# Kernel optimization log

Hardware: AMD Instinct MI355X
Metric: run time of the kernel (lower is better)

The kernel has to match this reference:

```python
import jax, jax.numpy as jnp
import numpy as np

BS, S, D, H, HS, HSEL, L = 32, 512, 512, 8, 2, 4, 6
DK = D // H  # 64
HD = H - HS  # dynamic heads


def setup_inputs() -> dict:
    key = jax.random.key(0)
    ks = jax.random.split(key, 10)
    w = lambda k, shape: jax.random.normal(k, shape, dtype=jnp.float32) * 0.02
    return {
        'q_embed_data': jax.random.normal(ks[0], (BS, S, D), jnp.float32),
        'qa_embed_data': jax.random.normal(ks[1], (BS, S, D), jnp.float32),
        # stacked per-layer params (torch Linear convention: W[out,in], y = x@W.T+b)
        'Wq': w(ks[2], (L, D, D)), 'bq': jnp.zeros((L, D), jnp.float32),
        'Wv': w(ks[3], (L, D, D)), 'bv': jnp.zeros((L, D), jnp.float32),
        'Wg': w(ks[4], (L, HD, D)),                      # routing gate, no bias
        'Wo': w(ks[5], (L, D, D)), 'bo': jnp.zeros((L, D), jnp.float32),
        'ln1_g': jnp.ones((L, D), jnp.float32), 'ln1_b': jnp.zeros((L, D), jnp.float32),
        'W1': w(ks[6], (L, D, D)), 'b1': jnp.zeros((L, D), jnp.float32),
        'W2': w(ks[7], (L, D, D)), 'b2': jnp.zeros((L, D), jnp.float32),
        'ln2_g': jnp.ones((L, D), jnp.float32), 'ln2_b': jnp.zeros((L, D), jnp.float32),
    }


def _layer_norm(x, g, b):
    m = x.mean(-1, keepdims=True)
    v = ((x - m) ** 2).mean(-1, keepdims=True)
    return (x - m) * jax.lax.rsqrt(v + 1e-5) * g + b


def _moh_attention(xq, xv, Wq, bq, Wv, bv, Wg, Wo, bo, strict):
    bs, s, d = xq.shape
    q = xq @ Wq.T + bq            # kq_same=True: k = q projection
    v = xv @ Wv.T + bv
    qh = q.reshape(bs, s, H, DK).transpose(0, 2, 1, 3)   # [b,h,s,dk]
    vh = v.reshape(bs, s, H, DK).transpose(0, 2, 1, 3)
    scores = jnp.einsum('bhqd,bhkd->bhqk', qh, qh) / jnp.sqrt(jnp.float32(DK))
    # mask==1 -> causal incl. diag; mask==0 -> strictly causal
    allow = jnp.tril(jnp.ones((s, s), bool), k=-1 if strict else 0)
    scores = jnp.where(allow, scores, jnp.float32(-1e9))
    # pad-zero shift: first query row replaced by zeros -> uniform attention
    scores = scores.at[:, :, 0, :].set(0.0)
    # per-token top-k head routing over dynamic heads
    gates = jax.nn.softmax(q.reshape(bs * s, D) @ Wg.T, axis=-1)  # [bs*s, HD]
    _, idx = jax.lax.top_k(gates, HSEL)
    dmask = jnp.zeros_like(gates).at[jnp.arange(bs * s)[:, None], idx].set(1.0)
    dyn = (gates * dmask).reshape(bs, s, HD)
    routing = jnp.concatenate([jnp.ones((bs, s, HS), gates.dtype), dyn], -1).mean(1)  # [b,H]
    attn = jax.nn.softmax(scores, axis=-1)
    ctx = jnp.einsum('bhqk,bhkd->bhqd', attn, vh) * routing[:, :, None, None]
    out = ctx.transpose(0, 2, 1, 3).reshape(bs, s, D) @ Wo.T + bo
    f = dmask.sum(0)
    P = gates.mean(0)
    balance = jnp.sum((f / (f.sum() + 1e-5)) * (P / (P.sum() + 1e-5)))
    return out, balance


def reference(q_embed_data, qa_embed_data, Wq, bq, Wv, bv, Wg, Wo, bo,
              ln1_g, ln1_b, W1, b1, W2, b2, ln2_g, ln2_b):
    def layer(i, xq, xv, strict):
        a, bl = _moh_attention(xq, xv, Wq[i], bq[i], Wv[i], bv[i], Wg[i], Wo[i], bo[i], strict)
        x = _layer_norm(xq + a, ln1_g[i], ln1_b[i])
        ffn = jax.nn.relu(x @ W1[i].T + b1[i]) @ W2[i].T + b2[i]
        return _layer_norm(x + ffn, ln2_g[i], ln2_b[i]), bl

    y = qa_embed_data
    x = q_embed_data
    # blocks_1: self-attention on y, mask=1
    y, _ = layer(0, y, y, False)
    y, _ = layer(1, y, y, False)
    # blocks_2: alternate mask=1 self-attn / mask=0 cross-attn (values=y)
    x, _ = layer(2, x, x, False)
    x, bl = layer(3, x, y, True)
    x, _ = layer(4, x, x, False)
    x, bl = layer(5, x, y, True)
    return (x, bl)
```

## Files before the change

kernel.cpp:

```cpp
#include <hip/hip_runtime.h>
#include <cstdint>

#define BSZ 32
#define SEQ 512
#define DM  512
#define NH  8
#define DK  64
#define HS_ 2
#define HD_ 6
#define NL  6
#define MROWS (BSZ*SEQ)
#define QVLD 1024
#define SCL 0.18033688011112043f

typedef unsigned short bf16_t;
typedef __attribute__((ext_vector_type(4))) float f32x4;
typedef __attribute__((ext_vector_type(8))) short bf16x8;
typedef __attribute__((ext_vector_type(8))) unsigned short u16x8;

#define DEV static __device__ __forceinline__

DEV float bf2f(bf16_t b) {
  unsigned int u = ((unsigned int)b) << 16;
  float f; __builtin_memcpy(&f, &u, 4); return f;
}
DEV bf16_t f2b(float f) {
  unsigned int u; __builtin_memcpy(&u, &f, 4);
  unsigned int r = (u + 0x7fffu + ((u >> 16) & 1u)) >> 16;
  return (bf16_t)r;
}
DEV void unp2(unsigned int w, float& a, float& b) {
  unsigned int ua = w << 16, ub = w & 0xffff0000u;
  __builtin_memcpy(&a, &ua, 4); __builtin_memcpy(&b, &ub, 4);
}
DEV unsigned cvtpk(float lo, float hi) {
  unsigned r;
  asm("v_cvt_pk_bf16_f32 %0, %1, %2" : "=v"(r) : "v"(lo), "v"(hi));
  return r;
}

DEV void gload_lds16(const bf16_t* g, bf16_t* l) {
  __builtin_amdgcn_global_load_lds(
      (const __attribute__((address_space(1))) void*)g,
      (__attribute__((address_space(3))) void*)l, 16, 0, 0);
}

DEV bf16x8 scale_q(bf16x8 v) {
  u16x8 u;
  __builtin_memcpy(&u, &v, 16);
  unsigned w[4];
#pragma unroll
  for (int e = 0; e < 4; ++e)
    w[e] = cvtpk(bf2f(u[2 * e]) * SCL, bf2f(u[2 * e + 1]) * SCL);
  bf16x8 r;
  __builtin_memcpy(&r, w, 16);
  return r;
}

__global__ __launch_bounds__(256) void f2b2_kernel(
    const float* __restrict__ s0, const float* __restrict__ s1,
    bf16_t* __restrict__ d0, bf16_t* __restrict__ d1) {
  const float* s = blockIdx.y ? s1 : s0;
  bf16_t* d = blockIdx.y ? d1 : d0;
  const int i = blockIdx.x * 256 + threadIdx.x;
  float4 v = reinterpret_cast<const float4*>(s)[i];
  ushort4 o;
  o.x = f2b(v.x); o.y = f2b(v.y); o.z = f2b(v.z); o.w = f2b(v.w);
  reinterpret_cast<ushort4*>(d)[i] = o;
}

__global__ __launch_bounds__(256) void f2bw_kernel(
    const float* __restrict__ s0, const float* __restrict__ s1,
    const float* __restrict__ s2, const float* __restrict__ s3,
    const float* __restrict__ s4, bf16_t* __restrict__ dst) {
  const float* srcs[5] = {s0, s1, s2, s3, s4};
  const float* s = srcs[blockIdx.y];
  bf16_t* d = dst + (size_t)blockIdx.y * ((size_t)NL * DM * DM);
  const int i = blockIdx.x * 256 + threadIdx.x;
  float4 v = reinterpret_cast<const float4*>(s)[i];
  ushort4 o;
  o.x = f2b(v.x); o.y = f2b(v.y); o.z = f2b(v.z); o.w = f2b(v.w);
  reinterpret_cast<ushort4*>(d)[i] = o;
}

__global__ __launch_bounds__(256) void gemm_qv(
    const bf16_t* __restrict__ A0, const bf16_t* __restrict__ A1,
    const bf16_t* __restrict__ W0, const bf16_t* __restrict__ W1,
    const float* __restrict__ b0, const float* __restrict__ b1,
    bf16_t* __restrict__ Yb) {
  const int K = 512;
  const int lin = blockIdx.y * 8 + blockIdx.x;
  const int swz = (lin & 7) * 128 + (lin >> 3);
  const int bn = swz & 7, bm = swz >> 3;
  const int tid = threadIdx.x, wid = tid >> 6, lane = tid & 63;
  const int wr = wid >> 1, wc = wid & 1;
  __shared__ __align__(16) bf16_t As[128 * 64];
  __shared__ __align__(16) bf16_t Bs[128 * 64];

  const bool hi = bn >= 4;
  const bf16_t* Asel = hi ? A1 : A0;
  const bf16_t* Wsel = hi ? (W1 - (size_t)512 * K) : W0;
  const float* bsel = hi ? (b1 - 512) : b0;

  f32x4 acc[4][4];
#pragma unroll
  for (int m = 0; m < 4; ++m)
#pragma unroll
    for (int n = 0; n < 4; ++n) acc[m][n] = f32x4{0.f, 0.f, 0.f, 0.f};

  const int lrow = lane & 15, lko = (lane >> 4) * 8;
  const int sr = wid * 8 + (lane >> 3), scol = (lane & 7) * 8;
  const size_t arow0 = (size_t)bm * 128, brow0 = (size_t)bn * 128;

  for (int k0 = 0; k0 < K; k0 += 64) {
#pragma unroll
    for (int i = 0; i < 4; ++i) {
      gload_lds16(Asel + (arow0 + i * 32 + sr) * K + k0 + scol, &As[(i * 4 + wid) * 512]);
      gload_lds16(Wsel + (brow0 + i * 32 + sr) * K + k0 + scol, &Bs[(i * 4 + wid) * 512]);
    }
    __syncthreads();
    bf16x8 af[4][2], bw[4][2];
#pragma unroll
    for (int m = 0; m < 4; ++m)
#pragma unroll
      for (int ks = 0; ks < 2; ++ks)
        af[m][ks] = *reinterpret_cast<const bf16x8*>(
            &As[(wr * 64 + m * 16 + lrow) * 64 + ks * 32 + lko]);
#pragma unroll
    for (int n = 0; n < 4; ++n)
#pragma unroll
      for (int ks = 0; ks < 2; ++ks)
        bw[n][ks] = *reinterpret_cast<const bf16x8*>(
            &Bs[(wc * 64 + n * 16 + lrow) * 64 + ks * 32 + lko]);
    __builtin_amdgcn_s_setprio(1);
#pragma unroll
    for (int ks = 0; ks < 2; ++ks)
#pragma unroll
      for (int m = 0; m < 4; ++m)
#pragma unroll
        for (int n = 0; n < 4; ++n)
          acc[m][n] = __builtin_amdgcn_mfma_f32_16x16x32_bf16(af[m][ks], bw[n][ks], acc[m][n], 0, 0, 0);
    __builtin_amdgcn_s_setprio(0);
    __syncthreads();
  }

  const int r0 = bm * 128 + wr * 64 + (lane >> 4) * 4;
  const int c0 = bn * 128 + wc * 64 + lrow;
#pragma unroll
  for (int n = 0; n < 4; ++n) {
    const int col = c0 + n * 16;
    const float bc = bsel[col];
#pragma unroll
    for (int m = 0; m < 4; ++m)
#pragma unroll
      for (int j = 0; j < 4; ++j)
        Yb[(size_t)(r0 + m * 16 + j) * QVLD + col] = f2b(acc[m][n][j] + bc);
  }
}

template <bool RELU>
__global__ __launch_bounds__(256) void gemm_n512(
    const bf16_t* __restrict__ A, const bf16_t* __restrict__ W,
    const float* __restrict__ bias, bf16_t* __restrict__ Yb) {
  const int K = 512;
  const int lin = blockIdx.y * 4 + blockIdx.x;
  const int swz = (lin & 7) * 128 + (lin >> 3);
  const int bn = swz & 3, bm = swz >> 2;
  const int tid = threadIdx.x, wid = tid >> 6, lane = tid & 63;
  const int wr = wid >> 1, wc = wid & 1;
  __shared__ __align__(16) bf16_t As[64 * 64];
  __shared__ __align__(16) bf16_t Bs[128 * 64];

  f32x4 acc[2][4];
#pragma unroll
  for (int m = 0; m < 2; ++m)
#pragma unroll
    for (int n = 0; n < 4; ++n) acc[m][n] = f32x4{0.f, 0.f, 0.f, 0.f};

  const int lrow = lane & 15, lko = (lane >> 4) * 8;
  const int sr = wid * 8 + (lane >> 3), scol = (lane & 7) * 8;
  const size_t arow0 = (size_t)bm * 64, brow0 = (size_t)bn * 128;

  for (int k0 = 0; k0 < K; k0 += 64) {
#pragma unroll
    for (int i = 0; i < 2; ++i)
      gload_lds16(A + (arow0 + i * 32 + sr) * K + k0 + scol, &As[(i * 4 + wid) * 512]);
#pragma unroll
    for (int i = 0; i < 4; ++i)
      gload_lds16(W + (brow0 + i * 32 + sr) * K + k0 + scol, &Bs[(i * 4 + wid) * 512]);
    __syncthreads();
    bf16x8 af[2][2], bw[4][2];
#pragma unroll
    for (int m = 0; m < 2; ++m)
#pragma unroll
      for (int ks = 0; ks < 2; ++ks)
        af[m][ks] = *reinterpret_cast<const bf16x8*>(
            &As[(wr * 32 + m * 16 + lrow) * 64 + ks * 32 + lko]);
#pragma unroll
    for (int n = 0; n < 4; ++n)
#pragma unroll
      for (int ks = 0; ks < 2; ++ks)
        bw[n][ks] = *reinterpret_cast<const bf16x8*>(
            &Bs[(wc * 64 + n * 16 + lrow) * 64 + ks * 32 + lko]);
    __builtin_amdgcn_s_setprio(1);
#pragma unroll
    for (int ks = 0; ks < 2; ++ks)
#pragma unroll
      for (int m = 0; m < 2; ++m)
#pragma unroll
        for (int n = 0; n < 4; ++n)
          acc[m][n] = __builtin_amdgcn_mfma_f32_16x16x32_bf16(af[m][ks], bw[n][ks], acc[m][n], 0, 0, 0);
    __builtin_amdgcn_s_setprio(0);
    __syncthreads();
  }

  const int r0 = bm * 64 + wr * 32 + (lane >> 4) * 4;
  const int c0 = bn * 128 + wc * 64 + lrow;
#pragma unroll
  for (int n = 0; n < 4; ++n) {
    const int col = c0 + n * 16;
    const float bc = bias[col];
#pragma unroll
    for (int m = 0; m < 2; ++m)
#pragma unroll
      for (int j = 0; j < 4; ++j) {
        float v = acc[m][n][j] + bc;
        if (RELU) v = fmaxf(v, 0.f);
        Yb[(size_t)(r0 + m * 16 + j) * DM + col] = f2b(v);
      }
  }
}

__global__ __launch_bounds__(256) void gates_kernel(
    const bf16_t* __restrict__ qv, const float* __restrict__ Wg,
    float* __restrict__ rdyn, float* __restrict__ fP) {
  __shared__ float wg_s[HD_ * DM];
  __shared__ float blk[4][18];
  const int tid = threadIdx.x, wid = tid >> 6, lane = tid & 63;
  for (int i = tid; i < HD_ * DM / 4; i += 256)
    reinterpret_cast<float4*>(wg_s)[i] = reinterpret_cast<const float4*>(Wg)[i];
  __syncthreads();
  const int bb = blockIdx.x >> 3;
  const int t0 = (blockIdx.x & 7) * 64 + wid * 16;
  float fs[6] = {0, 0, 0, 0, 0, 0}, ps[6] = {0, 0, 0, 0, 0, 0}, rs[6] = {0, 0, 0, 0, 0, 0};
  for (int it = 0; it < 16; ++it) {
    const int tok = bb * SEQ + t0 + it;
    uint4 u = reinterpret_cast<const uint4*>(qv + (size_t)tok * QVLD)[lane];
    float x[8];
    unp2(u.x, x[0], x[1]); unp2(u.y, x[2], x[3]);
    unp2(u.z, x[4], x[5]); unp2(u.w, x[6], x[7]);
    float g[6];
#pragma unroll
    for (int j = 0; j < 6; ++j) {
      float p = 0.f;
#pragma unroll
      for (int e = 0; e < 8; ++e) p = fmaf(x[e], wg_s[j * DM + lane * 8 + e], p);
#pragma unroll
      for (int off = 32; off; off >>= 1) p += __shfl_xor(p, off);
      g[j] = p;
    }
    float mx = g[0];
#pragma unroll
    for (int j = 1; j < 6; ++j) mx = fmaxf(mx, g[j]);
    float se = 0.f;
#pragma unroll
    for (int j = 0; j < 6; ++j) { g[j] = __expf(g[j] - mx); se += g[j]; }
    float inv = 1.f / se;
#pragma unroll
    for (int j = 0; j < 6; ++j) g[j] *= inv;
    int d1 = 0;
#pragma unroll
    for (int j = 1; j < 6; ++j)
      if (g[j] < g[d1] || (g[j] == g[d1] && j > d1)) d1 = j;
    int d2 = (d1 == 0) ? 1 : 0;
#pragma unroll
    for (int j = 0; j < 6; ++j) {
      if (j == d1) continue;
      if (g[j] < g[d2] || (g[j] == g[d2] && j > d2)) d2 = j;
    }
#pragma unroll
    for (int j = 0; j < 6; ++j) {
      const bool drop = (j == d1) || (j == d2);
      fs[j] += drop ? 0.f : 1.f;
      ps[j] += g[j];
      rs[j] += drop ? 0.f : g[j];
    }
  }
  if (lane == 0) {
#pragma unroll
    for (int j = 0; j < 6; ++j) {
      blk[wid][j] = fs[j]; blk[wid][6 + j] = ps[j]; blk[wid][12 + j] = rs[j];
    }
  }
  __syncthreads();
  if (tid < 18) {
    float s = blk[0][tid] + blk[1][tid] + blk[2][tid] + blk[3][tid];
    if (tid < 12) atomicAdd(&fP[tid], s);
    else atomicAdd(&rdyn[bb * 6 + (tid - 12)], s * (1.f / 512.f));
  }
}

__global__ __launch_bounds__(256, 2) void fattn_kernel(
    const bf16_t* __restrict__ qv, const float* __restrict__ rdyn,
    bf16_t* __restrict__ ctx, int strict) {
  const int lin = (blockIdx.z * 8 + blockIdx.y) * 2 + blockIdx.x;
  const int swz = (lin & 7) * 64 + (lin >> 3);
  const int bx = swz & 1, h = (swz >> 1) & 7, b = swz >> 4;
  const int tid = threadIdx.x, wid = tid >> 6, lane = tid & 63;
  const int c0 = lane & 15, grp = lane >> 4;
  const int l3 = lane >> 3, c3 = lane & 7;
  const int kidx = lane & 31, dhalf = lane >> 5;

  __shared__ __align__(16) bf16_t Ks[64 * 64];
  __shared__ __align__(16) bf16_t Vt[64 * 72];
  __shared__ __align__(16) bf16_t Ps[4][32 * 64];
  __shared__ float csum[64];

  const bf16_t* qp = qv;
  const bf16_t* vp = qv + 512;
  const float factor = (h < HS_) ? 1.f : rdyn[b * 6 + (h - HS_)];

  const int qtA = bx, qtB = 3 - bx;
  const int qbaseA = qtA * 128 + wid * 32;
  const int qbaseB = qtB * 128 + wid * 32;

  bf16x8 qfA[2][2], qfB[2][2];
#pragma unroll
  for (int nt = 0; nt < 2; ++nt)
#pragma unroll
    for (int ks = 0; ks < 2; ++ks) {
      qfA[nt][ks] = scale_q(*reinterpret_cast<const bf16x8*>(
          qp + ((size_t)(b * SEQ + qbaseA + nt * 16 + c0)) * QVLD + h * DK + ks * 32 + grp * 8));
      qfB[nt][ks] = scale_q(*reinterpret_cast<const bf16x8*>(
          qp + ((size_t)(b * SEQ + qbaseB + nt * 16 + c0)) * QVLD + h * DK + ks * 32 + grp * 8));
    }

  f32x4 accA[2][4], accB[2][4];
#pragma unroll
  for (int m = 0; m < 2; ++m)
#pragma unroll
    for (int d = 0; d < 4; ++d) {
      accA[m][d] = f32x4{0.f, 0.f, 0.f, 0.f};
      accB[m][d] = f32x4{0.f, 0.f, 0.f, 0.f};
    }
  float mA[2] = {-3e38f, -3e38f}, lA[2] = {0.f, 0.f};
  float mB[2] = {-3e38f, -3e38f}, lB[2] = {0.f, 0.f};
  float cs[8] = {0, 0, 0, 0, 0, 0, 0, 0};

  const int lastA = (qbaseA + 31 - strict) >> 6;
  const int lastB = (qbaseB + 31 - strict) >> 6;
  const int ktmax = 2 * qtB + 1;

  auto do_tile = [&](bf16x8 (&qf)[2][2], f32x4 (&acc)[2][4], float (&mreg)[2],
                     float (&lreg)[2], int qbase, bool masked, int kt) {
    const char* KsB = (const char*)Ks;
    bf16x8 kf[4][2];
#pragma unroll
    for (int mt = 0; mt < 4; ++mt)
#pragma unroll
      for (int ks = 0; ks < 2; ++ks)
        kf[mt][ks] = *reinterpret_cast<const bf16x8*>(
            KsB + (mt * 16 + c0) * 128 + 16 * ((4 * ks + grp) ^ (c0 & 7)));
    f32x4 s[4][2];
#pragma unroll
    for (int mt = 0; mt < 4; ++mt)
#pragma unroll
      for (int nt = 0; nt < 2; ++nt) s[mt][nt] = f32x4{0.f, 0.f, 0.f, 0.f};
    __builtin_amdgcn_s_setprio(1);
#pragma unroll
    for (int mt = 0; mt < 4; ++mt)
#pragma unroll
      for (int nt = 0; nt < 2; ++nt)
#pragma unroll
        for (int ks = 0; ks < 2; ++ks)
          s[mt][nt] = __builtin_amdgcn_mfma_f32_16x16x32_bf16(
              kf[mt][ks], qf[nt][ks], s[mt][nt], 0, 0, 0);
    __builtin_amdgcn_s_setprio(0);

    if (masked) {
#pragma unroll
      for (int nt = 0; nt < 2; ++nt) {
        const int q = qbase + nt * 16 + c0;
#pragma unroll
        for (int mt = 0; mt < 4; ++mt)
#pragma unroll
          for (int j = 0; j < 4; ++j) {
            int k = kt * 64 + mt * 16 + grp * 4 + j;
            if (k + strict > q) s[mt][nt][j] = -1e30f;
          }
      }
    }
    float mx[2];
#pragma unroll
    for (int nt = 0; nt < 2; ++nt) {
      float a = fmaxf(s[0][nt][0], s[0][nt][1]);
      a = fmaxf(fmaxf(a, s[0][nt][2]), s[0][nt][3]);
      float bm_ = fmaxf(s[1][nt][0], s[1][nt][1]);
      bm_ = fmaxf(fmaxf(bm_, s[1][nt][2]), s[1][nt][3]);
      float c = fmaxf(s[2][nt][0], s[2][nt][1]);
      c = fmaxf(fmaxf(c, s[2][nt][2]), s[2][nt][3]);
      float d = fmaxf(s[3][nt][0], s[3][nt][1]);
      d = fmaxf(fmaxf(d, s[3][nt][2]), s[3][nt][3]);
      float m_ = fmaxf(fmaxf(a, bm_), fmaxf(c, d));
      m_ = fmaxf(m_, __shfl_xor(m_, 16));
      m_ = fmaxf(m_, __shfl_xor(m_, 32));
      mx[nt] = m_;
    }
    const bool defer = __all((mx[0] - mreg[0] <= 8.f) && (mx[1] - mreg[1] <= 8.f));
    float sc[2];
#pragma unroll
    for (int nt = 0; nt < 2; ++nt) {
      const float mnew = defer ? mreg[nt] : fmaxf(mreg[nt], mx[nt]);
      float ts = 0.f;
#pragma unroll
      for (int mt = 0; mt < 4; ++mt)
#pragma unroll
        for (int j = 0; j < 4; ++j) {
          float pp = exp2f(s[mt][nt][j] - mnew);
          s[mt][nt][j] = pp; ts += pp;
        }
      ts += __shfl_xor(ts, 16);
      ts += __shfl_xor(ts, 32);
      if (defer) {
        lreg[nt] += ts;
      } else {
        sc[nt] = exp2f(mreg[nt] - mnew);
        lreg[nt] = lreg[nt] * sc[nt] + ts;
        mreg[nt] = mnew;
      }
    }
    char* PsB = (char*)(&Ps[wid][0]);
#pragma unroll
    for (int nt = 0; nt < 2; ++nt)
#pragma unroll
      for (int mt = 0; mt < 4; ++mt) {
        uint2 w;
        w.x = cvtpk(s[mt][nt][0], s[mt][nt][1]);
        w.y = cvtpk(s[mt][nt][2], s[mt][nt][3]);
        int row = nt * 16 + c0;
        int off = (row * 128 + mt * 32 + grp * 8) ^ ((c0 & 7) << 4);
        *reinterpret_cast<uint2*>(PsB + off) = w;
      }
    if (!defer) {
#pragma unroll
      for (int mtq = 0; mtq < 2; ++mtq) {
        f32x4 sv;
#pragma unroll
        for (int j = 0; j < 4; ++j) sv[j] = __shfl(sc[mtq], grp * 4 + j);
#pragma unroll
        for (int dt = 0; dt < 4; ++dt) acc[mtq][dt] *= sv;
      }
    }
    bf16x8 pf[2][2], vf2[4][2];
#pragma unroll
    for (int mtq = 0; mtq < 2; ++mtq)
#pragma unroll
      for (int ks = 0; ks < 2; ++ks)
        pf[mtq][ks] = *reinterpret_cast<const bf16x8*>(
            PsB + (mtq * 16 + c0) * 128 + 16 * ((4 * ks + grp) ^ (c0 & 7)));
#pragma unroll
    for (int dt = 0; dt < 4; ++dt)
#pragma unroll
      for (int ks = 0; ks < 2; ++ks)
        vf2[dt][ks] = *reinterpret_cast<const bf16x8*>(
            (const char*)Vt + (dt * 16 + c0) * 144 + ks * 64 + grp * 16);
    __builtin_amdgcn_s_setprio(1);
#pragma unroll
    for (int mtq = 0; mtq < 2; ++mtq)
#pragma unroll
      for (int dt = 0; dt < 4; ++dt)
#pragma unroll
        for (int ks = 0; ks < 2; ++ks)
          acc[mtq][dt] = __builtin_amdgcn_mfma_f32_16x16x32_bf16(
              pf[mtq][ks], vf2[dt][ks], acc[mtq][dt], 0, 0, 0);
    __builtin_amdgcn_s_setprio(0);
  };

  for (int kt = 0; kt <= ktmax; ++kt) {
#pragma unroll
    for (int i = 0; i < 2; ++i) {
      int row = i * 32 + wid * 8 + l3;
      int blk = c3 ^ l3;
      gload_lds16(qp + ((size_t)(b * SEQ + kt * 64 + row)) * QVLD + h * DK + blk * 8,
                  Ks + (i * 32 + wid * 8) * 64);
    }
#pragma unroll
    for (int j = 0; j < 2; ++j) {
      const int d0 = (wid * 2 + j) * 8 + dhalf * 4;
      const bf16_t* src = vp + ((size_t)(b * SEQ + kt * 64 + 2 * kidx)) * QVLD + h * DK + d0;
      ushort4 lo = *reinterpret_cast<const ushort4*>(src);
      ushort4 hv = *reinterpret_cast<const ushort4*>(src + QVLD);
      *reinterpret_cast<unsigned*>(&Vt[(d0 + 0) * 72 + 2 * kidx]) = (unsigned)lo.x | ((unsigned)hv.x << 16);
      *reinterpret_cast<unsigned*>(&Vt[(d0 + 1) * 72 + 2 * kidx]) = (unsigned)lo.y | ((unsigned)hv.y << 16);
      *reinterpret_cast<unsigned*>(&Vt[(d0 + 2) * 72 + 2 * kidx]) = (unsigned)lo.z | ((unsigned)hv.z << 16);
      *reinterpret_cast<unsigned*>(&Vt[(d0 + 3) * 72 + 2 * kidx]) = (unsigned)lo.w | ((unsigned)hv.w << 16);
      if (bx == 0) {
        cs[j * 4 + 0] += bf2f(lo.x) + bf2f(hv.x);
        cs[j * 4 + 1] += bf2f(lo.y) + bf2f(hv.y);
        cs[j * 4 + 2] += bf2f(lo.z) + bf2f(hv.z);
        cs[j * 4 + 3] += bf2f(lo.w) + bf2f(hv.w);
      }
    }
    __syncthreads();
    if (kt <= lastB) do_tile(qfB, accB, mB, lB, qbaseB, kt == lastB, kt);
    if (kt <= lastA) do_tile(qfA, accA, mA, lA, qbaseA, kt == lastA, kt);
    __syncthreads();
  }

  if (bx == 0) {
#pragma unroll
    for (int e = 0; e < 8; ++e)
#pragma unroll
      for (int off = 1; off <= 16; off <<= 1) cs[e] += __shfl_xor(cs[e], off);
    if ((lane & 31) == 0) {
#pragma unroll
      for (int e = 0; e < 8; ++e)
        csum[(wid * 2 + (e >> 2)) * 8 + dhalf * 4 + (e & 3)] = cs[e];
    }
  }
  __syncthreads();
  if (bx == 0 && tid < 64)
    ctx[((size_t)(b * SEQ)) * DM + h * DK + tid] = f2b(csum[tid] * (1.f / 512.f) * factor);

#pragma unroll
  for (int e = 0; e < 2; ++e) {
    const int qbase = e ? qbaseB : qbaseA;
    f32x4 (&acc)[2][4] = e ? accB : accA;
    float (&lreg)[2] = e ? lB : lA;
#pragma unroll
    for (int mtq = 0; mtq < 2; ++mtq) {
      const float inv = factor / lreg[mtq];
      f32x4 iv;
#pragma unroll
      for (int j = 0; j < 4; ++j) iv[j] = __shfl(inv, grp * 4 + j);
#pragma unroll
      for (int j = 0; j < 4; ++j) {
        const int q = qbase + mtq * 16 + grp * 4 + j;
        if (q == 0) continue;
#pragma unroll
        for (int dt = 0; dt < 4; ++dt)
          ctx[((size_t)(b * SEQ + q)) * DM + h * DK + dt * 16 + c0] =
              f2b(acc[mtq][dt][j] * iv[j]);
      }
    }
  }
}

template <int OUT>
__global__ __launch_bounds__(256) void add_ln_kernel(
    const bf16_t* __restrict__ X, const bf16_t* __restrict__ A2,
    const float* __restrict__ gam, const float* __restrict__ bet,
    bf16_t* __restrict__ outb, float* __restrict__ outf) {
  const int wid = threadIdx.x >> 6, lane = threadIdx.x & 63;
  const size_t row = (size_t)blockIdx.x * 4 + wid;
  const size_t base = row * DM + lane * 8;
  uint4 xu = *reinterpret_cast<const uint4*>(X + base);
  uint4 au = *reinterpret_cast<const uint4*>(A2 + base);
  float z[8];
  {
    float p0, p1, q0, q1;
    unp2(xu.x, p0, p1); unp2(au.x, q0, q1); z[0] = p0 + q0; z[1] = p1 + q1;
    unp2(xu.y, p0, p1); unp2(au.y, q0, q1); z[2] = p0 + q0; z[3] = p1 + q1;
    unp2(xu.z, p0, p1); unp2(au.z, q0, q1); z[4] = p0 + q0; z[5] = p1 + q1;
    unp2(xu.w, p0, p1); unp2(au.w, q0, q1); z[6] = p0 + q0; z[7] = p1 + q1;
  }
  float s = 0.f;
#pragma unroll
  for (int e = 0; e < 8; ++e) s += z[e];
#pragma unroll
  for (int off = 32; off; off >>= 1) s += __shfl_xor(s, off);
  const float mean = s * (1.f / 512.f);
  float ss = 0.f;
#pragma unroll
  for (int e = 0; e < 8; ++e) { float d = z[e] - mean; ss += d * d; }
#pragma unroll
  for (int off = 32; off; off >>= 1) ss += __shfl_xor(ss, off);
  const float inv = rsqrtf(ss * (1.f / 512.f) + 1e-5f);
  float4 g0 = *reinterpret_cast<const float4*>(gam + lane * 8);
  float4 g1 = *reinterpret_cast<const float4*>(gam + lane * 8 + 4);
  float4 b0 = *reinterpret_cast<const float4*>(bet + lane * 8);
  float4 b1 = *reinterpret_cast<const float4*>(bet + lane * 8 + 4);
  float o[8];
  o[0] = (z[0] - mean) * inv * g0.x + b0.x;
  o[1] = (z[1] - mean) * inv * g0.y + b0.y;
  o[2] = (z[2] - mean) * inv * g0.z + b0.z;
  o[3] = (z[3] - mean) * inv * g0.w + b0.w;
  o[4] = (z[4] - mean) * inv * g1.x + b1.x;
  o[5] = (z[5] - mean) * inv * g1.y + b1.y;
  o[6] = (z[6] - mean) * inv * g1.z + b1.z;
  o[7] = (z[7] - mean) * inv * g1.w + b1.w;
  if (OUT == 0) {
    uint4 w;
    w.x = (unsigned)f2b(o[0]) | ((unsigned)f2b(o[1]) << 16);
    w.y = (unsigned)f2b(o[2]) | ((unsigned)f2b(o[3]) << 16);
    w.z = (unsigned)f2b(o[4]) | ((unsigned)f2b(o[5]) << 16);
    w.w = (unsigned)f2b(o[6]) | ((unsigned)f2b(o[7]) << 16);
    *reinterpret_cast<uint4*>(outb + base) = w;
  } else {
    float4 f0, f1;
    f0.x = o[0]; f0.y = o[1]; f0.z = o[2]; f0.w = o[3];
    f1.x = o[4]; f1.y = o[5]; f1.z = o[6]; f1.w = o[7];
    *reinterpret_cast<float4*>(outf + base) = f0;
    *reinterpret_cast<float4*>(outf + base + 4) = f1;
  }
}

__global__ void balance_kernel(const float* __restrict__ fP, float* __restrict__ out) {
  if (threadIdx.x == 0 && blockIdx.x == 0) {
    float fs = 0.f, pssum = 0.f, P[6];
    for (int j = 0; j < 6; ++j) {
      fs += fP[j];
      P[j] = fP[6 + j] * (1.f / (float)MROWS);
      pssum += P[j];
    }
    float bal = 0.f;
    for (int j = 0; j < 6; ++j)
      bal += (fP[j] / (fs + 1e-5f)) * (P[j] / (pssum + 1e-5f));
    out[0] = bal;
  }
}

extern "C" void kernel_launch(void* const* d_in, const int* in_sizes, int n_in,
                              void* d_out, int out_size, void* d_ws, size_t ws_size,
                              hipStream_t stream) {
  (void)in_sizes; (void)n_in; (void)out_size; (void)ws_size;
  const float* q_embed  = (const float*)d_in[0];
  const float* qa_embed = (const float*)d_in[1];
  const float* Wq  = (const float*)d_in[2];
  const float* bq  = (const float*)d_in[3];
  const float* Wv  = (const float*)d_in[4];
  const float* bv  = (const float*)d_in[5];
  const float* Wg  = (const float*)d_in[6];
  const float* Wo  = (const float*)d_in[7];
  const float* bo  = (const float*)d_in[8];
  const float* ln1g = (const float*)d_in[9];
  const float* ln1b = (const float*)d_in[10];
  const float* W1  = (const float*)d_in[11];
  const float* b1  = (const float*)d_in[12];
  const float* W2  = (const float*)d_in[13];
  const float* b2  = (const float*)d_in[14];
  const float* ln2g = (const float*)d_in[15];
  const float* ln2b = (const float*)d_in[16];

  char* p = (char*)d_ws;
  auto alloc = [&](size_t bytes) -> char* {
    char* r = p; p += (bytes + 255) & ~(size_t)255; return r;
  };
  const size_t WDE = (size_t)NL * DM * DM;
  const size_t AE  = (size_t)MROWS * DM;
  bf16_t* wall_b = (bf16_t*)alloc(5 * WDE * 2);
  bf16_t* wq_b = wall_b;
  bf16_t* wv_b = wall_b + WDE;
  bf16_t* wo_b = wall_b + 2 * WDE;
  bf16_t* w1_b = wall_b + 3 * WDE;
  bf16_t* w2_b = wall_b + 4 * WDE;
  bf16_t* y_b   = (bf16_t*)alloc(AE * 2);
  bf16_t* x_b   = (bf16_t*)alloc(AE * 2);
  bf16_t* qv_b  = (bf16_t*)alloc((size_t)MROWS * QVLD * 2);
  bf16_t* ctx_b = (bf16_t*)alloc(AE * 2);
  bf16_t* x1_b  = (bf16_t*)alloc(AE * 2);
  bf16_t* tmp_b = (bf16_t*)alloc(AE * 2);
  bf16_t* ffn1_b = (bf16_t*)alloc(AE * 2);
  float* stats = (float*)alloc(NL * (12 + BSZ * 6) * 4);
  float* fPbase = stats;
  float* rdynbase = stats + NL * 12;

  hipMemsetAsync(stats, 0, NL * (12 + BSZ * 6) * 4, stream);

  f2bw_kernel<<<dim3((unsigned)(WDE / 4 / 256), 5), 256, 0, stream>>>(
      Wq, Wv, Wo, W1, W2, wall_b);
  f2b2_kernel<<<dim3((unsigned)(AE / 4 / 256), 2), 256, 0, stream>>>(
      qa_embed, q_embed, y_b, x_b);

  const size_t DD = (size_t)DM * DM;
  dim3 gqv(8, 128), gn5(4, 256);
  float* outx = (float*)d_out;

  auto layer = [&](int i, bf16_t* resb, const bf16_t* xvb, int strict, bool last) {
    float* fP = fPbase + i * 12;
    float* rdyn = rdynbase + i * (BSZ * 6);
    gemm_qv<<<gqv, 256, 0, stream>>>(
        resb, xvb, wq_b + i * DD, wv_b + i * DD, bq + i * DM, bv + i * DM, qv_b);
    gates_kernel<<<MROWS / 64, 256, 0, stream>>>(qv_b, Wg + (size_t)i * HD_ * DM, rdyn, fP);
    fattn_kernel<<<dim3(2, NH, BSZ), 256, 0, stream>>>(qv_b, rdyn, ctx_b, strict);
    gemm_n512<false><<<gn5, 256, 0, stream>>>(ctx_b, wo_b + i * DD, bo + i * DM, tmp_b);
    add_ln_kernel<0><<<MROWS / 4, 256, 0, stream>>>(
        resb, tmp_b, ln1g + i * DM, ln1b + i * DM, x1_b, nullptr);
    gemm_n512<true><<<gn5, 256, 0, stream>>>(x1_b, w1_b + i * DD, b1 + i * DM, ffn1_b);
    gemm_n512<false><<<gn5, 256, 0, stream>>>(ffn1_b, w2_b + i * DD, b2 + i * DM, tmp_b);
    if (last)
      add_ln_kernel<1><<<MROWS / 4, 256, 0, stream>>>(
          x1_b, tmp_b, ln2g + i * DM, ln2b + i * DM, nullptr, outx);
    else
      add_ln_kernel<0><<<MROWS / 4, 256, 0, stream>>>(
          x1_b, tmp_b, ln2g + i * DM, ln2b + i * DM, resb, nullptr);
  };

  layer(0, y_b, y_b, 0, false);
  layer(1, y_b, y_b, 0, false);
  layer(2, x_b, x_b, 0, false);
  layer(3, x_b, y_b, 1, false);
  layer(4, x_b, x_b, 0, false);
  layer(5, x_b, y_b, 1, true);
  balance_kernel<<<1, 64, 0, stream>>>(fPbase + 5 * 12, outx + (size_t)MROWS * DM);
}
```

Baseline: 1.013 ms.

## Split attention into one block per query tile and halve gates block work

The attention kernel used to pair query tiles (t and 3-t) in one block to balance causal work across 512 blocks. It now launches 1024 blocks, one per query tile, each loading K/V only up to its own causal extent. The column-sum for the zero row moves to the qt==3 block. The gates kernel also uses twice as many blocks with half the tokens each. This adds parallelism and shrinks the per-block register footprint, at the cost of load imbalance across blocks and redundant K/V loads between tiles of the same head.

```diff
diff --git a/kernel.cpp b/kernel.cpp
--- a/kernel.cpp
+++ b/kernel.cpp
@@ -240,10 +240,10 @@
   for (int i = tid; i < HD_ * DM / 4; i += 256)
     reinterpret_cast<float4*>(wg_s)[i] = reinterpret_cast<const float4*>(Wg)[i];
   __syncthreads();
-  const int bb = blockIdx.x >> 3;
-  const int t0 = (blockIdx.x & 7) * 64 + wid * 16;
+  const int bb = blockIdx.x >> 4;
+  const int t0 = (blockIdx.x & 15) * 32 + wid * 8;
   float fs[6] = {0, 0, 0, 0, 0, 0}, ps[6] = {0, 0, 0, 0, 0, 0}, rs[6] = {0, 0, 0, 0, 0, 0};
-  for (int it = 0; it < 16; ++it) {
+  for (int it = 0; it < 8; ++it) {
     const int tok = bb * SEQ + t0 + it;
     uint4 u = reinterpret_cast<const uint4*>(qv + (size_t)tok * QVLD)[lane];
     float x[8];
@@ -303,9 +303,8 @@
 __global__ __launch_bounds__(256, 2) void fattn_kernel(
     const bf16_t* __restrict__ qv, const float* __restrict__ rdyn,
     bf16_t* __restrict__ ctx, int strict) {
-  const int lin = (blockIdx.z * 8 + blockIdx.y) * 2 + blockIdx.x;
-  const int swz = (lin & 7) * 64 + (lin >> 3);
-  const int bx = swz & 1, h = (swz >> 1) & 7, b = swz >> 4;
+  const int bh = blockIdx.x, qt = blockIdx.y;
+  const int b = bh >> 3, h = bh & 7;
   const int tid = threadIdx.x, wid = tid >> 6, lane = tid & 63;
   const int c0 = lane & 15, grp = lane >> 4;
   const int l3 = lane >> 3, c3 = lane & 7;
@@ -320,161 +319,27 @@
   const bf16_t* vp = qv + 512;
   const float factor = (h < HS_) ? 1.f : rdyn[b * 6 + (h - HS_)];
 
-  const int qtA = bx, qtB = 3 - bx;
-  const int qbaseA = qtA * 128 + wid * 32;
-  const int qbaseB = qtB * 128 + wid * 32;
-
-  bf16x8 qfA[2][2], qfB[2][2];
+  const int qbase = qt * 128 + wid * 32;
+
+  bf16x8 qf[2][2];
 #pragma unroll
   for (int nt = 0; nt < 2; ++nt)
 #pragma unroll
-    for (int ks = 0; ks < 2; ++ks) {
-      qfA[nt][ks] = scale_q(*reinterpret_cast<const bf16x8*>(
-          qp + ((size_t)(b * SEQ + qbaseA + nt * 16 + c0)) * QVLD + h * DK + ks * 32 + grp * 8));
-      qfB[nt][ks] = scale_q(*reinterpret_cast<const bf16x8*>(
-          qp + ((size_t)(b * SEQ + qbaseB + nt * 16 + c0)) * QVLD + h * DK + ks * 32 + grp * 8));
-    }
-
-  f32x4 accA[2][4], accB[2][4];
+    for (int ks = 0; ks < 2; ++ks)
+      qf[nt][ks] = scale_q(*reinterpret_cast<const bf16x8*>(
+          qp + ((size_t)(b * SEQ + qbase + nt * 16 + c0)) * QVLD + h * DK + ks * 32 + grp * 8));
+
+  f32x4 acc[2][4];
 #pragma unroll
   for (int m = 0; m < 2; ++m)
 #pragma unroll
-    for (int d = 0; d < 4; ++d) {
-      accA[m][d] = f32x4{0.f, 0.f, 0.f, 0.f};
-      accB[m][d] = f32x4{0.f, 0.f, 0.f, 0.f};
-    }
-  float mA[2] = {-3e38f, -3e38f}, lA[2] = {0.f, 0.f};
-  float mB[2] = {-3e38f, -3e38f}, lB[2] = {0.f, 0.f};
+    for (int d = 0; d < 4; ++d) acc[m][d] = f32x4{0.f, 0.f, 0.f, 0.f};
+  float mreg[2] = {-3e38f, -3e38f};
+  float lreg[2] = {0.f, 0.f};
   float cs[8] = {0, 0, 0, 0, 0, 0, 0, 0};
 
-  const int lastA = (qbaseA + 31 - strict) >> 6;
-  const int lastB = (qbaseB + 31 - strict) >> 6;
-  const int ktmax = 2 * qtB + 1;
-
-  auto do_tile = [&](bf16x8 (&qf)[2][2], f32x4 (&acc)[2][4], float (&mreg)[2],
-                     float (&lreg)[2], int qbase, bool masked, int kt) {
-    const char* KsB = (const char*)Ks;
-    bf16x8 kf[4][2];
-#pragma unroll
-    for (int mt = 0; mt < 4; ++mt)
-#pragma unroll
-      for (int ks = 0; ks < 2; ++ks)
-        kf[mt][ks] = *reinterpret_cast<const bf16x8*>(
-            KsB + (mt * 16 + c0) * 128 + 16 * ((4 * ks + grp) ^ (c0 & 7)));
-    f32x4 s[4][2];
-#pragma unroll
-    for (int mt = 0; mt < 4; ++mt)
-#pragma unroll
-      for (int nt = 0; nt < 2; ++nt) s[mt][nt] = f32x4{0.f, 0.f, 0.f, 0.f};
-    __builtin_amdgcn_s_setprio(1);
-#pragma unroll
-    for (int mt = 0; mt < 4; ++mt)
-#pragma unroll
-      for (int nt = 0; nt < 2; ++nt)
-#pragma unroll
-        for (int ks = 0; ks < 2; ++ks)
-          s[mt][nt] = __builtin_amdgcn_mfma_f32_16x16x32_bf16(
-              kf[mt][ks], qf[nt][ks], s[mt][nt], 0, 0, 0);
-    __builtin_amdgcn_s_setprio(0);
-
-    if (masked) {
-#pragma unroll
-      for (int nt = 0; nt < 2; ++nt) {
-        const int q = qbase + nt * 16 + c0;
-#pragma unroll
-        for (int mt = 0; mt < 4; ++mt)
-#pragma unroll
-          for (int j = 0; j < 4; ++j) {
-            int k = kt * 64 + mt * 16 + grp * 4 + j;
-            if (k + strict > q) s[mt][nt][j] = -1e30f;
-          }
-      }
-    }
-    float mx[2];
-#pragma unroll
-    for (int nt = 0; nt < 2; ++nt) {
-      float a = fmaxf(s[0][nt][0], s[0][nt][1]);
-      a = fmaxf(fmaxf(a, s[0][nt][2]), s[0][nt][3]);
-      float bm_ = fmaxf(s[1][nt][0], s[1][nt][1]);
-      bm_ = fmaxf(fmaxf(bm_, s[1][nt][2]), s[1][nt][3]);
-      float c = fmaxf(s[2][nt][0], s[2][nt][1]);
-      c = fmaxf(fmaxf(c, s[2][nt][2]), s[2][nt][3]);
-      float d = fmaxf(s[3][nt][0], s[3][nt][1]);
-      d = fmaxf(fmaxf(d, s[3][nt][2]), s[3][nt][3]);
-      float m_ = fmaxf(fmaxf(a, bm_), fmaxf(c, d));
-      m_ = fmaxf(m_, __shfl_xor(m_, 16));
-      m_ = fmaxf(m_, __shfl_xor(m_, 32));
-      mx[nt] = m_;
-    }
-    const bool defer = __all((mx[0] - mreg[0] <= 8.f) && (mx[1] - mreg[1] <= 8.f));
-    float sc[2];
-#pragma unroll
-    for (int nt = 0; nt < 2; ++nt) {
-      const float mnew = defer ? mreg[nt] : fmaxf(mreg[nt], mx[nt]);
-      float ts = 0.f;
-#pragma unroll
-      for (int mt = 0; mt < 4; ++mt)
-#pragma unroll
-        for (int j = 0; j < 4; ++j) {
-          float pp = exp2f(s[mt][nt][j] - mnew);
-          s[mt][nt][j] = pp; ts += pp;
-        }
-      ts += __shfl_xor(ts, 16);
-      ts += __shfl_xor(ts, 32);
-      if (defer) {
-        lreg[nt] += ts;
-      } else {
-        sc[nt] = exp2f(mreg[nt] - mnew);
-        lreg[nt] = lreg[nt] * sc[nt] + ts;
-        mreg[nt] = mnew;
-      }
-    }
-    char* PsB = (char*)(&Ps[wid][0]);
-#pragma unroll
-    for (int nt = 0; nt < 2; ++nt)
-#pragma unroll
-      for (int mt = 0; mt < 4; ++mt) {
-        uint2 w;
-        w.x = cvtpk(s[mt][nt][0], s[mt][nt][1]);
-        w.y = cvtpk(s[mt][nt][2], s[mt][nt][3]);
-        int row = nt * 16 + c0;
-        int off = (row * 128 + mt * 32 + grp * 8) ^ ((c0 & 7) << 4);
-        *reinterpret_cast<uint2*>(PsB + off) = w;
-      }
-    if (!defer) {
-#pragma unroll
-      for (int mtq = 0; mtq < 2; ++mtq) {
-        f32x4 sv;
-#pragma unroll
-        for (int j = 0; j < 4; ++j) sv[j] = __shfl(sc[mtq], grp * 4 + j);
-#pragma unroll
-        for (int dt = 0; dt < 4; ++dt) acc[mtq][dt] *= sv;
-      }
-    }
-    bf16x8 pf[2][2], vf2[4][2];
-#pragma unroll
-    for (int mtq = 0; mtq < 2; ++mtq)
-#pragma unroll
-      for (int ks = 0; ks < 2; ++ks)
-        pf[mtq][ks] = *reinterpret_cast<const bf16x8*>(
-            PsB + (mtq * 16 + c0) * 128 + 16 * ((4 * ks + grp) ^ (c0 & 7)));
-#pragma unroll
-    for (int dt = 0; dt < 4; ++dt)
-#pragma unroll
-      for (int ks = 0; ks < 2; ++ks)
-        vf2[dt][ks] = *reinterpret_cast<const bf16x8*>(
-            (const char*)Vt + (dt * 16 + c0) * 144 + ks * 64 + grp * 16);
-    __builtin_amdgcn_s_setprio(1);
-#pragma unroll
-    for (int mtq = 0; mtq < 2; ++mtq)
-#pragma unroll
-      for (int dt = 0; dt < 4; ++dt)
-#pragma unroll
-        for (int ks = 0; ks < 2; ++ks)
-          acc[mtq][dt] = __builtin_amdgcn_mfma_f32_16x16x32_bf16(
-              pf[mtq][ks], vf2[dt][ks], acc[mtq][dt], 0, 0, 0);
-    __builtin_amdgcn_s_setprio(0);
-  };
+  const int lastk = (qbase + 31 - strict) >> 6;
+  const int ktmax = 2 * qt + 1;
 
   for (int kt = 0; kt <= ktmax; ++kt) {
 #pragma unroll
@@ -494,7 +359,7 @@
       *reinterpret_cast<unsigned*>(&Vt[(d0 + 1) * 72 + 2 * kidx]) = (unsigned)lo.y | ((unsigned)hv.y << 16);
       *reinterpret_cast<unsigned*>(&Vt[(d0 + 2) * 72 + 2 * kidx]) = (unsigned)lo.z | ((unsigned)hv.z << 16);
       *reinterpret_cast<unsigned*>(&Vt[(d0 + 3) * 72 + 2 * kidx]) = (unsigned)lo.w | ((unsigned)hv.w << 16);
-      if (bx == 0) {
+      if (qt == 3) {
         cs[j * 4 + 0] += bf2f(lo.x) + bf2f(hv.x);
         cs[j * 4 + 1] += bf2f(lo.y) + bf2f(hv.y);
         cs[j * 4 + 2] += bf2f(lo.z) + bf2f(hv.z);
@@ -502,12 +367,135 @@
       }
     }
     __syncthreads();
-    if (kt <= lastB) do_tile(qfB, accB, mB, lB, qbaseB, kt == lastB, kt);
-    if (kt <= lastA) do_tile(qfA, accA, mA, lA, qbaseA, kt == lastA, kt);
+
+    if (kt <= lastk) {
+      const char* KsB = (const char*)Ks;
+      bf16x8 kf[4][2];
+#pragma unroll
+      for (int mt = 0; mt < 4; ++mt)
+#pragma unroll
+        for (int ks = 0; ks < 2; ++ks)
+          kf[mt][ks] = *reinterpret_cast<const bf16x8*>(
+              KsB + (mt * 16 + c0) * 128 + 16 * ((4 * ks + grp) ^ (c0 & 7)));
+      f32x4 s[4][2];
+#pragma unroll
+      for (int mt = 0; mt < 4; ++mt)
+#pragma unroll
+        for (int nt = 0; nt < 2; ++nt) s[mt][nt] = f32x4{0.f, 0.f, 0.f, 0.f};
+      __builtin_amdgcn_s_setprio(1);
+#pragma unroll
+      for (int mt = 0; mt < 4; ++mt)
+#pragma unroll
+        for (int nt = 0; nt < 2; ++nt)
+#pragma unroll
+          for (int ks = 0; ks < 2; ++ks)
+            s[mt][nt] = __builtin_amdgcn_mfma_f32_16x16x32_bf16(
+                kf[mt][ks], qf[nt][ks], s[mt][nt], 0, 0, 0);
+      __builtin_amdgcn_s_setprio(0);
+
+      const bool masked = (kt == lastk);
+      if (masked) {
+#pragma unroll
+        for (int nt = 0; nt < 2; ++nt) {
+          const int q = qbase + nt * 16 + c0;
+#pragma unroll
+          for (int mt = 0; mt < 4; ++mt)
+#pragma unroll
+            for (int j = 0; j < 4; ++j) {
+              int k = kt * 64 + mt * 16 + grp * 4 + j;
+              if (k + strict > q) s[mt][nt][j] = -1e30f;
+            }
+        }
+      }
+      float mx[2];
+#pragma unroll
+      for (int nt = 0; nt < 2; ++nt) {
+        float a = fmaxf(s[0][nt][0], s[0][nt][1]);
+        a = fmaxf(fmaxf(a, s[0][nt][2]), s[0][nt][3]);
+        float bm_ = fmaxf(s[1][nt][0], s[1][nt][1]);
+        bm_ = fmaxf(fmaxf(bm_, s[1][nt][2]), s[1][nt][3]);
+        float c = fmaxf(s[2][nt][0], s[2][nt][1]);
+        c = fmaxf(fmaxf(c, s[2][nt][2]), s[2][nt][3]);
+        float d = fmaxf(s[3][nt][0], s[3][nt][1]);
+        d = fmaxf(fmaxf(d, s[3][nt][2]), s[3][nt][3]);
+        float m_ = fmaxf(fmaxf(a, bm_), fmaxf(c, d));
+        m_ = fmaxf(m_, __shfl_xor(m_, 16));
+        m_ = fmaxf(m_, __shfl_xor(m_, 32));
+        mx[nt] = m_;
+      }
+      const bool defer = __all((mx[0] - mreg[0] <= 8.f) && (mx[1] - mreg[1] <= 8.f));
+      float sc[2];
+#pragma unroll
+      for (int nt = 0; nt < 2; ++nt) {
+        const float mnew = defer ? mreg[nt] : fmaxf(mreg[nt], mx[nt]);
+        float ts = 0.f;
+#pragma unroll
+        for (int mt = 0; mt < 4; ++mt)
+#pragma unroll
+          for (int j = 0; j < 4; ++j) {
+            float pp = exp2f(s[mt][nt][j] - mnew);
+            s[mt][nt][j] = pp; ts += pp;
+          }
+        ts += __shfl_xor(ts, 16);
+        ts += __shfl_xor(ts, 32);
+        if (defer) {
+          lreg[nt] += ts;
+        } else {
+          sc[nt] = exp2f(mreg[nt] - mnew);
+          lreg[nt] = lreg[nt] * sc[nt] + ts;
+          mreg[nt] = mnew;
+        }
+      }
+      char* PsB = (char*)(&Ps[wid][0]);
+#pragma unroll
+      for (int nt = 0; nt < 2; ++nt)
+#pragma unroll
+        for (int mt = 0; mt < 4; ++mt) {
+          uint2 w;
+          w.x = cvtpk(s[mt][nt][0], s[mt][nt][1]);
+          w.y = cvtpk(s[mt][nt][2], s[mt][nt][3]);
+          int row = nt * 16 + c0;
+          int off = (row * 128 + mt * 32 + grp * 8) ^ ((c0 & 7) << 4);
+          *reinterpret_cast<uint2*>(PsB + off) = w;
+        }
+      if (!defer) {
+#pragma unroll
+        for (int mtq = 0; mtq < 2; ++mtq) {
+          f32x4 sv;
+#pragma unroll
+          for (int j = 0; j < 4; ++j) sv[j] = __shfl(sc[mtq], grp * 4 + j);
+#pragma unroll
+          for (int dt = 0; dt < 4; ++dt) acc[mtq][dt] *= sv;
+        }
+      }
+      bf16x8 pf[2][2], vf2[4][2];
+#pragma unroll
+      for (int mtq = 0; mtq < 2; ++mtq)
+#pragma unroll
+        for (int ks = 0; ks < 2; ++ks)
+          pf[mtq][ks] = *reinterpret_cast<const bf16x8*>(
+              PsB + (mtq * 16 + c0) * 128 + 16 * ((4 * ks + grp) ^ (c0 & 7)));
+#pragma unroll
+      for (int dt = 0; dt < 4; ++dt)
+#pragma unroll
+        for (int ks = 0; ks < 2; ++ks)
+          vf2[dt][ks] = *reinterpret_cast<const bf16x8*>(
+              (const char*)Vt + (dt * 16 + c0) * 144 + ks * 64 + grp * 16);
+      __builtin_amdgcn_s_setprio(1);
+#pragma unroll
+      for (int mtq = 0; mtq < 2; ++mtq)
+#pragma unroll
+        for (int dt = 0; dt < 4; ++dt)
+#pragma unroll
+          for (int ks = 0; ks < 2; ++ks)
+            acc[mtq][dt] = __builtin_amdgcn_mfma_f32_16x16x32_bf16(
+                pf[mtq][ks], vf2[dt][ks], acc[mtq][dt], 0, 0, 0);
+      __builtin_amdgcn_s_setprio(0);
+    }
     __syncthreads();
   }
 
-  if (bx == 0) {
+  if (qt == 3) {
 #pragma unroll
     for (int e = 0; e < 8; ++e)
 #pragma unroll
@@ -517,31 +505,25 @@
       for (int e = 0; e < 8; ++e)
         csum[(wid * 2 + (e >> 2)) * 8 + dhalf * 4 + (e & 3)] = cs[e];
     }
-  }
-  __syncthreads();
-  if (bx == 0 && tid < 64)
-    ctx[((size_t)(b * SEQ)) * DM + h * DK + tid] = f2b(csum[tid] * (1.f / 512.f) * factor);
-
-#pragma unroll
-  for (int e = 0; e < 2; ++e) {
-    const int qbase = e ? qbaseB : qbaseA;
-    f32x4 (&acc)[2][4] = e ? accB : accA;
-    float (&lreg)[2] = e ? lB : lA;
-#pragma unroll
-    for (int mtq = 0; mtq < 2; ++mtq) {
-      const float inv = factor / lreg[mtq];
-      f32x4 iv;
-#pragma unroll
-      for (int j = 0; j < 4; ++j) iv[j] = __shfl(inv, grp * 4 + j);
-#pragma unroll
-      for (int j = 0; j < 4; ++j) {
-        const int q = qbase + mtq * 16 + grp * 4 + j;
-        if (q == 0) continue;
-#pragma unroll
-        for (int dt = 0; dt < 4; ++dt)
-          ctx[((size_t)(b * SEQ + q)) * DM + h * DK + dt * 16 + c0] =
-              f2b(acc[mtq][dt][j] * iv[j]);
-      }
+    __syncthreads();
+    if (tid < 64)
+      ctx[((size_t)(b * SEQ)) * DM + h * DK + tid] = f2b(csum[tid] * (1.f / 512.f) * factor);
+  }
+
+#pragma unroll
+  for (int mtq = 0; mtq < 2; ++mtq) {
+    const float inv = factor / lreg[mtq];
+    f32x4 iv;
+#pragma unroll
+    for (int j = 0; j < 4; ++j) iv[j] = __shfl(inv, grp * 4 + j);
+#pragma unroll
+    for (int j = 0; j < 4; ++j) {
+      const int q = qbase + mtq * 16 + grp * 4 + j;
+      if (q == 0) continue;
+#pragma unroll
+      for (int dt = 0; dt < 4; ++dt)
+        ctx[((size_t)(b * SEQ + q)) * DM + h * DK + dt * 16 + c0] =
+            f2b(acc[mtq][dt][j] * iv[j]);
     }
   }
 }
@@ -673,7 +655,7 @@
       qa_embed, q_embed, y_b, x_b);
 
   const size_t DD = (size_t)DM * DM;
-  dim3 gqv(8, 128), gn5(4, 256);
+  dim3 gqv(8, 128), gn5(4, 256), gfa(256, 4);
   float* outx = (float*)d_out;
 
   auto layer = [&](int i, bf16_t* resb, const bf16_t* xvb, int strict, bool last) {
@@ -681,8 +663,8 @@
     float* rdyn = rdynbase + i * (BSZ * 6);
     gemm_qv<<<gqv, 256, 0, stream>>>(
         resb, xvb, wq_b + i * DD, wv_b + i * DD, bq + i * DM, bv + i * DM, qv_b);
-    gates_kernel<<<MROWS / 64, 256, 0, stream>>>(qv_b, Wg + (size_t)i * HD_ * DM, rdyn, fP);
-    fattn_kernel<<<dim3(2, NH, BSZ), 256, 0, stream>>>(qv_b, rdyn, ctx_b, strict);
+    gates_kernel<<<MROWS / 32, 256, 0, stream>>>(qv_b, Wg + (size_t)i * HD_ * DM, rdyn, fP);
+    fattn_kernel<<<gfa, 256, 0, stream>>>(qv_b, rdyn, ctx_b, strict);
     gemm_n512<false><<<gn5, 256, 0, stream>>>(ctx_b, wo_b + i * DD, bo + i * DM, tmp_b);
     add_ln_kernel<0><<<MROWS / 4, 256, 0, stream>>>(
         resb, tmp_b, ln1g + i * DM, ln1b + i * DM, x1_b, nullptr);
```

Measured after the change: 969.3 us. -4.3%, faster.
